# Optimization experiments

Measured on AMD Instinct MI355X. Metric: run time of the kernel, lower is better.

## Reference

```python
import jax, jax.numpy as jnp
import numpy as np

B, S, D, H = 4, 2048, 1024, 16
LOOKAHEAD, LEFT_CTX = 64, 512


def setup_inputs() -> dict:
    key = jax.random.key(0)
    k1, k2, k3, k4, k5 = jax.random.split(key, 5)
    scale = 1.0 / np.sqrt(D)
    return {
        "x": jax.random.normal(k1, (B, S, D), dtype=jnp.float32),
        "W_in": jax.random.normal(k2, (3 * D, D), dtype=jnp.float32) * scale,
        "b_in": jax.random.normal(k3, (3 * D,), dtype=jnp.float32) * 0.02,
        "W_out": jax.random.normal(k4, (D, D), dtype=jnp.float32) * scale,
        "b_out": jax.random.normal(k5, (D,), dtype=jnp.float32) * 0.02,
        "nhead": H,
        "lookahead": LOOKAHEAD,
        "left_context": LEFT_CTX,
    }


def reference(x, W_in, b_in, W_out, b_out, nhead, lookahead, left_context):
    b, s, d = x.shape
    hd = d // nhead
    # fused in-projection: [B,S,3D] -> q,k,v each [B,H,S,hd]
    qkv = x @ W_in.T + b_in
    q, k, v = jnp.split(qkv, 3, axis=-1)
    def heads(t):
        return t.reshape(b, s, nhead, hd).transpose(0, 2, 1, 3)
    q, k, v = heads(q), heads(k), heads(v)
    scores = jnp.einsum("bhqd,bhkd->bhqk", q, k) / jnp.sqrt(jnp.float32(hd))
    # banded causal+lookahead mask (every row has >=1 allowed entry)
    i = jnp.arange(s)[:, None]
    j = jnp.arange(s)[None, :]
    allowed = (j <= i + lookahead) & (j >= i - left_context)
    scores = jnp.where(allowed, scores, -jnp.inf)
    attn = jax.nn.softmax(scores, axis=-1)
    ctx = jnp.einsum("bhqk,bhkd->bhqd", attn, v)
    ctx = ctx.transpose(0, 2, 1, 3).reshape(b, s, d)
    return ctx @ W_out.T + b_out
```

## Files before the change

kernel.cpp:

```cpp
#include <hip/hip_runtime.h>
#include <hip/hip_fp16.h>

typedef _Float16 f16x4_t __attribute__((ext_vector_type(4)));
typedef _Float16 f16x8_t __attribute__((ext_vector_type(8)));
typedef float    f32x4_t __attribute__((ext_vector_type(4)));

#define GLDS16(gp, lp)                                                                   \
  __builtin_amdgcn_global_load_lds((const __attribute__((address_space(1))) void*)(gp),  \
                                   (__attribute__((address_space(3))) void*)(lp), 16, 0, 0)

constexpr int BB = 4, SS = 2048, DD = 1024, HH = 16, HDIM = 64;
constexpr int LOOKA = 64, LEFTC = 512;
constexpr int MROWS = BB * SS;
constexpr int N3D = 3 * DD;

__global__ void cvt_kernel(const float* __restrict__ in, _Float16* __restrict__ out) {
  const int i = (blockIdx.x * 256 + threadIdx.x) * 4;
  const float4 v = *reinterpret_cast<const float4*>(in + i);
  f16x4_t o;
  o[0] = (_Float16)v.x; o[1] = (_Float16)v.y; o[2] = (_Float16)v.z; o[3] = (_Float16)v.w;
  *reinterpret_cast<f16x4_t*>(out + i) = o;
}

template <bool OUT_F32>
__global__ void gemm_nt(const _Float16* __restrict__ A, const _Float16* __restrict__ Bm,
                        const float* __restrict__ bias, void* __restrict__ Cout,
                        const int N, const int K, const int ldc, _Float16* __restrict__ vt) {
  constexpr int BK = 64;
  __shared__ _Float16 As[128 * BK];
  __shared__ _Float16 Bs[128 * BK];
  const int tid = threadIdx.x;
  const int wid = tid >> 6;
  const int lane = tid & 63;
  const int lr = lane & 15, lg = lane >> 4;
  const int wr = wid >> 1, wc = wid & 1;
  const size_t arow0 = (size_t)blockIdx.x * 128;
  const size_t bcol0 = (size_t)blockIdx.y * 128;

  f32x4_t acc[4][4] = {};

  const int srow = wid * 32 + (lane >> 3);
  const int scol = (lane & 7) * 8;
  const _Float16* Ag = A + (arow0 + srow) * (size_t)K + scol;
  const _Float16* Bg = Bm + (bcol0 + srow) * (size_t)K + scol;

  for (int kt = 0; kt < K; kt += BK) {
    __syncthreads();
#pragma unroll
    for (int c = 0; c < 4; ++c) {
      GLDS16(Ag + kt + (size_t)(c * 8) * K, &As[(wid * 32 + c * 8) * BK]);
      GLDS16(Bg + kt + (size_t)(c * 8) * K, &Bs[(wid * 32 + c * 8) * BK]);
    }
    __syncthreads();
#pragma unroll
    for (int kk = 0; kk < 2; ++kk) {
      f16x8_t af[4], bf[4];
#pragma unroll
      for (int mi = 0; mi < 4; ++mi)
        af[mi] = *reinterpret_cast<const f16x8_t*>(&As[(wr * 64 + mi * 16 + lr) * BK + kk * 32 + lg * 8]);
#pragma unroll
      for (int ni = 0; ni < 4; ++ni)
        bf[ni] = *reinterpret_cast<const f16x8_t*>(&Bs[(wc * 64 + ni * 16 + lr) * BK + kk * 32 + lg * 8]);
#pragma unroll
      for (int mi = 0; mi < 4; ++mi)
#pragma unroll
        for (int ni = 0; ni < 4; ++ni)
          acc[mi][ni] = __builtin_amdgcn_mfma_f32_16x16x32_f16(af[mi], bf[ni], acc[mi][ni], 0, 0, 0);
    }
  }

  float bv[4];
#pragma unroll
  for (int ni = 0; ni < 4; ++ni) bv[ni] = bias[bcol0 + wc * 64 + ni * 16 + lr];

  if (!OUT_F32 && vt != nullptr && bcol0 >= 2048) {
#pragma unroll
    for (int mi = 0; mi < 4; ++mi)
#pragma unroll
      for (int ni = 0; ni < 4; ++ni) {
        const int col = (int)bcol0 + wc * 64 + ni * 16 + lr - 2048;
        const int hh = col >> 6, dd = col & 63;
        const size_t row = arow0 + wr * 64 + mi * 16 + lg * 4;
        const size_t bq = row >> 11, sq = row & 2047;
        f16x4_t o;
#pragma unroll
        for (int r = 0; r < 4; ++r) o[r] = (_Float16)(acc[mi][ni][r] + bv[ni]);
        *reinterpret_cast<f16x4_t*>(&vt[(((size_t)bq * HH + hh) * HDIM + dd) * SS + sq]) = o;
      }
  } else {
#pragma unroll
    for (int mi = 0; mi < 4; ++mi)
#pragma unroll
      for (int ni = 0; ni < 4; ++ni)
#pragma unroll
        for (int r = 0; r < 4; ++r) {
          const size_t row = arow0 + wr * 64 + mi * 16 + lg * 4 + r;
          const size_t col = bcol0 + wc * 64 + ni * 16 + lr;
          const float v = acc[mi][ni][r] + bv[ni];
          if (OUT_F32) ((float*)Cout)[row * ldc + col] = v;
          else         ((_Float16*)Cout)[row * ldc + col] = (_Float16)v;
        }
  }
}

__global__ void attn_kernel(const _Float16* __restrict__ qk, const _Float16* __restrict__ vt,
                            _Float16* __restrict__ ctx) {
  __shared__ _Float16 Ks[2][64 * 64];
  __shared__ _Float16 Vs[2][64 * 64];

  const int fid = blockIdx.x;
  const int nid = (fid & 7) * 256 + (fid >> 3);
  const int qt = nid & 31, h = (nid >> 5) & 15, b = nid >> 9;
  const int qs = qt * 64;
  const int tid = threadIdx.x, wid = tid >> 6, lane = tid & 63;
  const int lr = lane & 15, lg = lane >> 4;
  const int qrow0 = qs + wid * 16;

  const _Float16* qp = qk + (size_t)(b * SS + qrow0 + lr) * 2048 + h * HDIM + lg * 8;
  f16x8_t qf0 = *reinterpret_cast<const f16x8_t*>(qp);
  f16x8_t qf1 = *reinterpret_cast<const f16x8_t*>(qp + 32);
#pragma unroll
  for (int j = 0; j < 8; ++j) {
    qf0[j] = qf0[j] * (_Float16)0.125f;
    qf1[j] = qf1[j] * (_Float16)0.125f;
  }

  f32x4_t oaccT[4] = {};
  float lpart = 0.f;

  const int klo = max(0, qs - LEFTC);
  const int khi = min(SS, qs + 64 + LOOKA);
  const int nt = (khi - klo) >> 6;

  const int srow = lane >> 3;
  const int c16 = (lane & 7) ^ srow;
  const char* kbase = (const char*)qk + (size_t)(b * SS) * 4096 + 2048 + h * 128 + (size_t)c16 * 16;
  const char* vbase = (const char*)vt + ((size_t)(b * HH + h) * HDIM) * 4096 + (size_t)c16 * 16;

  auto stage = [&](int buf, int kt) {
#pragma unroll
    for (int i = 0; i < 2; ++i) {
      const int row = (wid * 2 + i) * 8 + srow;
      GLDS16(kbase + (size_t)(kt + row) * 4096, (char*)&Ks[buf][0] + (wid * 2 + i) * 1024);
      GLDS16(vbase + (size_t)row * 4096 + (size_t)kt * 2, (char*)&Vs[buf][0] + (wid * 2 + i) * 1024);
    }
  };

  stage(0, klo);
  __syncthreads();

  for (int t = 0; t < nt; ++t) {
    const int kt = klo + t * 64;
    const int cur = t & 1;
    if (t + 1 < nt) stage(cur ^ 1, klo + (t + 1) * 64);

    f32x4_t sacc[4] = {};
#pragma unroll
    for (int ki = 0; ki < 4; ++ki)
#pragma unroll
      for (int ks = 0; ks < 2; ++ks) {
        const f16x8_t kf = *reinterpret_cast<const f16x8_t*>(
            &Ks[cur][(ki * 16 + lr) * 64 + (((ks * 4 + lg) ^ (lr & 7)) * 8)]);
        sacc[ki] = __builtin_amdgcn_mfma_f32_16x16x32_f16(kf, ks == 0 ? qf0 : qf1, sacc[ki], 0, 0, 0);
      }

    const bool doMask = (t == 0 && qs >= LEFTC) || (t == nt - 1 && qs + 128 <= SS);
    if (doMask) {
      const int q = qrow0 + lr;
#pragma unroll
      for (int ki = 0; ki < 4; ++ki)
#pragma unroll
        for (int r = 0; r < 4; ++r) {
          const int key = kt + ki * 16 + lg * 4 + r;
          const bool ok = (key <= q + LOOKA) && (key + LEFTC >= q);
          sacc[ki][r] = ok ? sacc[ki][r] : -1e30f;
        }
    }

    f16x4_t pT[4];
#pragma unroll
    for (int ki = 0; ki < 4; ++ki)
#pragma unroll
      for (int r = 0; r < 4; ++r) {
        const float p = __expf(sacc[ki][r]);
        lpart += p;
        pT[ki][r] = (_Float16)p;
      }

#pragma unroll
    for (int ki = 0; ki < 4; ++ki)
#pragma unroll
      for (int di = 0; di < 4; ++di) {
        const f16x4_t vf = *reinterpret_cast<const f16x4_t*>(
            &Vs[cur][(di * 16 + lr) * 64 + ((((ki * 2 + (lg >> 1)) ^ (lr & 7)) << 3) + ((lg & 1) << 2))]);
        oaccT[di] = __builtin_amdgcn_mfma_f32_16x16x16f16(vf, pT[ki], oaccT[di], 0, 0, 0);
      }

    __syncthreads();
  }

  lpart += __shfl_xor(lpart, 16);
  lpart += __shfl_xor(lpart, 32);
  const float inv = 1.0f / lpart;
  const size_t orow = (size_t)(b * SS + qrow0 + lr) * DD + h * HDIM;
#pragma unroll
  for (int di = 0; di < 4; ++di) {
    f16x4_t o;
#pragma unroll
    for (int r = 0; r < 4; ++r) o[r] = (_Float16)(oaccT[di][r] * inv);
    *reinterpret_cast<f16x4_t*>(&ctx[orow + di * 16 + lg * 4]) = o;
  }
}

extern "C" void kernel_launch(void* const* d_in, const int* in_sizes, int n_in,
                              void* d_out, int out_size, void* d_ws, size_t ws_size,
                              hipStream_t stream) {
  const float* x     = (const float*)d_in[0];
  const float* W_in  = (const float*)d_in[1];
  const float* b_in  = (const float*)d_in[2];
  const float* W_out = (const float*)d_in[3];
  const float* b_out = (const float*)d_in[4];
  float* out = (float*)d_out;

  char* ws = (char*)d_ws;
  _Float16* xb   = (_Float16*)(ws);
  _Float16* wib  = (_Float16*)(ws + (16u << 20));
  _Float16* wob  = (_Float16*)(ws + (22u << 20));
  _Float16* qkb  = (_Float16*)(ws + (24u << 20));
  _Float16* ctxb = (_Float16*)(ws + (56u << 20));
  _Float16* vtb  = (_Float16*)(ws + (72u << 20));

  cvt_kernel<<<MROWS * DD / 1024, 256, 0, stream>>>(x, xb);
  cvt_kernel<<<N3D * DD / 1024, 256, 0, stream>>>(W_in, wib);
  cvt_kernel<<<DD * DD / 1024, 256, 0, stream>>>(W_out, wob);

  gemm_nt<false><<<dim3(MROWS / 128, N3D / 128), 256, 0, stream>>>(xb, wib, b_in, qkb, N3D, DD, 2048, vtb);
  attn_kernel<<<dim3(SS / 64 * HH * BB), 256, 0, stream>>>(qkb, vtb, ctxb);
  gemm_nt<true><<<dim3(MROWS / 128, DD / 128), 256, 0, stream>>>(ctxb, wob, b_out, out, DD, DD, DD, nullptr);
}
```

Baseline: 235.7 us.

## Replace QKV projection GEMM with 256x256 eight-wave pipelined MFMA kernel

Adds a dedicated QKV in-projection kernel that uses 256x256 output tiles, 8 waves, and double-buffered LDS. Each tile is split into quadrant phases, so async global-to-LDS loads for the next K step run alongside MFMA on the current one, using manual vmcnt waits, barriers and setprio. Blocks are remapped for L2 locality and LDS columns are XOR-swizzled. The aim is more reuse per loaded byte and better load/compute overlap than the 128x128 generic GEMM, at the cost of one block per CU and fragile hand-written synchronisation.

```diff
diff --git a/kernel.cpp b/kernel.cpp
--- a/kernel.cpp
+++ b/kernel.cpp
@@ -20,6 +20,175 @@
   f16x4_t o;
   o[0] = (_Float16)v.x; o[1] = (_Float16)v.y; o[2] = (_Float16)v.z; o[3] = (_Float16)v.w;
   *reinterpret_cast<f16x4_t*>(out + i) = o;
+}
+
+__global__ __launch_bounds__(512, 1) void gemm_qkv8(const _Float16* __restrict__ A,
+                                                    const _Float16* __restrict__ Bm,
+                                                    const float* __restrict__ bias,
+                                                    _Float16* __restrict__ Cout,
+                                                    _Float16* __restrict__ vt) {
+  constexpr int BK = 64, NT = 1024 / BK;
+  __shared__ _Float16 Ash[2][2][128 * 64];
+  __shared__ _Float16 Bsh[2][2][128 * 64];
+
+  const int bid = blockIdx.x;
+  const int nid = (bid & 7) * 48 + (bid >> 3);
+  const int mb = nid / 12, nb = nid % 12;
+  const size_t Mblk = (size_t)mb * 256, Nblk = (size_t)nb * 256;
+
+  const int tid = threadIdx.x;
+  const int w = tid >> 6, lane = tid & 63;
+  const int lr = lane & 15, lg = lane >> 4;
+  const int wr = w >> 2;
+  const int wc = w & 3;
+
+  const int rw = w * 8 + (lane >> 3);
+  const int cg = (lane & 7) ^ (lane >> 3);
+  const _Float16* Ag = A + (Mblk + rw) * 1024 + cg * 8;
+  const _Float16* Bg = Bm + (Nblk + rw) * 1024 + cg * 8;
+
+  auto stageA = [&](int t, int h) {
+    const int s = t & 1;
+    const int kt = (t & (NT - 1)) * BK;
+#pragma unroll
+    for (int i = 0; i < 2; ++i)
+      GLDS16(Ag + (size_t)(h * 128 + i * 64) * 1024 + kt,
+             (char*)&Ash[s][h][0] + w * 1024 + i * 8192);
+  };
+  auto stageB = [&](int t, int h) {
+    const int s = t & 1;
+    const int kt = (t & (NT - 1)) * BK;
+#pragma unroll
+    for (int i = 0; i < 2; ++i)
+      GLDS16(Bg + (size_t)(h * 128 + i * 64) * 1024 + kt,
+             (char*)&Bsh[s][h][0] + w * 1024 + i * 8192);
+  };
+
+  f32x4_t acc[2][4][2][2] = {};
+  f16x8_t af[4][2], bf0[2][2], bf1[2][2];
+
+  const int axr = (wr * 64 + lr) * 64;
+  const int bxr = (wc * 32 + lr) * 64;
+  const int c0 = (lg ^ (lr & 7)) * 8;
+  const int c1 = ((4 + lg) ^ (lr & 7)) * 8;
+
+  stageA(0, 0); stageB(0, 0); stageB(0, 1); stageA(0, 1);
+
+  for (int T = 0; T < NT; ++T) {
+    const int s = T & 1;
+    asm volatile("s_waitcnt vmcnt(4)" ::: "memory");
+    asm volatile("s_barrier" ::: "memory");
+#pragma unroll
+    for (int m = 0; m < 4; ++m) {
+      af[m][0] = *reinterpret_cast<const f16x8_t*>(&Ash[s][0][axr + m * 1024 + c0]);
+      af[m][1] = *reinterpret_cast<const f16x8_t*>(&Ash[s][0][axr + m * 1024 + c1]);
+    }
+#pragma unroll
+    for (int n = 0; n < 2; ++n) {
+      bf0[n][0] = *reinterpret_cast<const f16x8_t*>(&Bsh[s][0][bxr + n * 1024 + c0]);
+      bf0[n][1] = *reinterpret_cast<const f16x8_t*>(&Bsh[s][0][bxr + n * 1024 + c1]);
+    }
+    stageA(T + 1, 0);
+    __builtin_amdgcn_s_setprio(1);
+#pragma unroll
+    for (int m = 0; m < 4; ++m)
+#pragma unroll
+      for (int n = 0; n < 2; ++n)
+#pragma unroll
+        for (int kk = 0; kk < 2; ++kk)
+          acc[0][m][0][n] = __builtin_amdgcn_mfma_f32_16x16x32_f16(af[m][kk], bf0[n][kk], acc[0][m][0][n], 0, 0, 0);
+    __builtin_amdgcn_s_setprio(0);
+
+    asm volatile("s_waitcnt vmcnt(4)" ::: "memory");
+    asm volatile("s_barrier" ::: "memory");
+#pragma unroll
+    for (int n = 0; n < 2; ++n) {
+      bf1[n][0] = *reinterpret_cast<const f16x8_t*>(&Bsh[s][1][bxr + n * 1024 + c0]);
+      bf1[n][1] = *reinterpret_cast<const f16x8_t*>(&Bsh[s][1][bxr + n * 1024 + c1]);
+    }
+    stageB(T + 1, 0);
+    __builtin_amdgcn_s_setprio(1);
+#pragma unroll
+    for (int m = 0; m < 4; ++m)
+#pragma unroll
+      for (int n = 0; n < 2; ++n)
+#pragma unroll
+        for (int kk = 0; kk < 2; ++kk)
+          acc[0][m][1][n] = __builtin_amdgcn_mfma_f32_16x16x32_f16(af[m][kk], bf1[n][kk], acc[0][m][1][n], 0, 0, 0);
+    __builtin_amdgcn_s_setprio(0);
+
+    asm volatile("s_waitcnt vmcnt(4)" ::: "memory");
+    asm volatile("s_barrier" ::: "memory");
+#pragma unroll
+    for (int m = 0; m < 4; ++m) {
+      af[m][0] = *reinterpret_cast<const f16x8_t*>(&Ash[s][1][axr + m * 1024 + c0]);
+      af[m][1] = *reinterpret_cast<const f16x8_t*>(&Ash[s][1][axr + m * 1024 + c1]);
+    }
+    stageB(T + 1, 1);
+    __builtin_amdgcn_s_setprio(1);
+#pragma unroll
+    for (int m = 0; m < 4; ++m)
+#pragma unroll
+      for (int n = 0; n < 2; ++n)
+#pragma unroll
+        for (int kk = 0; kk < 2; ++kk)
+          acc[1][m][1][n] = __builtin_amdgcn_mfma_f32_16x16x32_f16(af[m][kk], bf1[n][kk], acc[1][m][1][n], 0, 0, 0);
+    __builtin_amdgcn_s_setprio(0);
+
+    asm volatile("s_barrier" ::: "memory");
+    stageA(T + 1, 1);
+    __builtin_amdgcn_s_setprio(1);
+#pragma unroll
+    for (int m = 0; m < 4; ++m)
+#pragma unroll
+      for (int n = 0; n < 2; ++n)
+#pragma unroll
+        for (int kk = 0; kk < 2; ++kk)
+          acc[1][m][0][n] = __builtin_amdgcn_mfma_f32_16x16x32_f16(af[m][kk], bf0[n][kk], acc[1][m][0][n], 0, 0, 0);
+    __builtin_amdgcn_s_setprio(0);
+  }
+
+  float bv[2][2];
+#pragma unroll
+  for (int nh = 0; nh < 2; ++nh)
+#pragma unroll
+    for (int n = 0; n < 2; ++n)
+      bv[nh][n] = bias[Nblk + nh * 128 + wc * 32 + n * 16 + lr];
+
+  if (nb >= 8) {
+#pragma unroll
+    for (int mh = 0; mh < 2; ++mh)
+#pragma unroll
+      for (int m = 0; m < 4; ++m)
+#pragma unroll
+        for (int nh = 0; nh < 2; ++nh)
+#pragma unroll
+          for (int n = 0; n < 2; ++n) {
+            const int col = (int)Nblk + nh * 128 + wc * 32 + n * 16 + lr - 2048;
+            const int hh = col >> 6, dd = col & 63;
+            const size_t row = Mblk + mh * 128 + wr * 64 + m * 16 + lg * 4;
+            const size_t bq = row >> 11, sq = row & 2047;
+            f16x4_t o;
+#pragma unroll
+            for (int r = 0; r < 4; ++r) o[r] = (_Float16)(acc[mh][m][nh][n][r] + bv[nh][n]);
+            *reinterpret_cast<f16x4_t*>(&vt[(((size_t)bq * HH + hh) * HDIM + dd) * SS + sq]) = o;
+          }
+  } else {
+#pragma unroll
+    for (int mh = 0; mh < 2; ++mh)
+#pragma unroll
+      for (int m = 0; m < 4; ++m)
+#pragma unroll
+        for (int nh = 0; nh < 2; ++nh)
+#pragma unroll
+          for (int n = 0; n < 2; ++n) {
+            const size_t col = Nblk + nh * 128 + wc * 32 + n * 16 + lr;
+            const size_t row0 = Mblk + mh * 128 + wr * 64 + m * 16 + lg * 4;
+#pragma unroll
+            for (int r = 0; r < 4; ++r)
+              Cout[(row0 + r) * 2048 + col] = (_Float16)(acc[mh][m][nh][n][r] + bv[nh][n]);
+          }
+  }
 }
 
 template <bool OUT_F32>
@@ -73,34 +242,18 @@
 #pragma unroll
   for (int ni = 0; ni < 4; ++ni) bv[ni] = bias[bcol0 + wc * 64 + ni * 16 + lr];
 
-  if (!OUT_F32 && vt != nullptr && bcol0 >= 2048) {
-#pragma unroll
-    for (int mi = 0; mi < 4; ++mi)
-#pragma unroll
-      for (int ni = 0; ni < 4; ++ni) {
-        const int col = (int)bcol0 + wc * 64 + ni * 16 + lr - 2048;
-        const int hh = col >> 6, dd = col & 63;
-        const size_t row = arow0 + wr * 64 + mi * 16 + lg * 4;
-        const size_t bq = row >> 11, sq = row & 2047;
-        f16x4_t o;
-#pragma unroll
-        for (int r = 0; r < 4; ++r) o[r] = (_Float16)(acc[mi][ni][r] + bv[ni]);
-        *reinterpret_cast<f16x4_t*>(&vt[(((size_t)bq * HH + hh) * HDIM + dd) * SS + sq]) = o;
+#pragma unroll
+  for (int mi = 0; mi < 4; ++mi)
+#pragma unroll
+    for (int ni = 0; ni < 4; ++ni)
+#pragma unroll
+      for (int r = 0; r < 4; ++r) {
+        const size_t row = arow0 + wr * 64 + mi * 16 + lg * 4 + r;
+        const size_t col = bcol0 + wc * 64 + ni * 16 + lr;
+        const float v = acc[mi][ni][r] + bv[ni];
+        if (OUT_F32) ((float*)Cout)[row * ldc + col] = v;
+        else         ((_Float16*)Cout)[row * ldc + col] = (_Float16)v;
       }
-  } else {
-#pragma unroll
-    for (int mi = 0; mi < 4; ++mi)
-#pragma unroll
-      for (int ni = 0; ni < 4; ++ni)
-#pragma unroll
-        for (int r = 0; r < 4; ++r) {
-          const size_t row = arow0 + wr * 64 + mi * 16 + lg * 4 + r;
-          const size_t col = bcol0 + wc * 64 + ni * 16 + lr;
-          const float v = acc[mi][ni][r] + bv[ni];
-          if (OUT_F32) ((float*)Cout)[row * ldc + col] = v;
-          else         ((_Float16*)Cout)[row * ldc + col] = (_Float16)v;
-        }
-  }
 }
 
 __global__ void attn_kernel(const _Float16* __restrict__ qk, const _Float16* __restrict__ vt,
@@ -234,7 +387,7 @@
   cvt_kernel<<<N3D * DD / 1024, 256, 0, stream>>>(W_in, wib);
   cvt_kernel<<<DD * DD / 1024, 256, 0, stream>>>(W_out, wob);
 
-  gemm_nt<false><<<dim3(MROWS / 128, N3D / 128), 256, 0, stream>>>(xb, wib, b_in, qkb, N3D, DD, 2048, vtb);
+  gemm_qkv8<<<dim3(32 * 12), 512, 0, stream>>>(xb, wib, b_in, qkb, vtb);
   attn_kernel<<<dim3(SS / 64 * HH * BB), 256, 0, stream>>>(qkb, vtb, ctxb);
   gemm_nt<true><<<dim3(MROWS / 128, DD / 128), 256, 0, stream>>>(ctxb, wob, b_out, out, DD, DD, DD, nullptr);
 }
```

New measurement: 235.0 us. Within noise of the previous version (-0.3%).
